# Performance work log

Measured on AMD Instinct MI355X. Metric: run time of the kernel, lower is better.

The kernel has to match this reference:

```python
import jax, jax.numpy as jnp
import numpy as np

EMBED_DIM = 1024
HIDDEN = 4 * EMBED_DIM
BATCH, SEQ = 4, 4096
EPS = 1e-5


def setup_inputs() -> dict:
    key = jax.random.key(0)
    k1, k2, k3 = jax.random.split(key, 3)
    x = jax.random.normal(k1, (BATCH, SEQ, EMBED_DIM), dtype=jnp.float32)
    # Kaiming-ish init scale for linear weights
    w1 = jax.random.normal(k2, (HIDDEN, EMBED_DIM), dtype=jnp.float32) * (1.0 / np.sqrt(EMBED_DIM))
    w2 = jax.random.normal(k3, (EMBED_DIM, HIDDEN), dtype=jnp.float32) * (1.0 / np.sqrt(HIDDEN))
    return {"x": x, "w1": w1, "w2": w2}


def _quant_weight(w):
    # BitNet-b1.58 absmean ternary quantization: clip(round(w/s), -1, 1) * s
    s = jnp.clip(jnp.mean(jnp.abs(w)), EPS, None)
    wq = jnp.clip(jnp.round(w / s), -1.0, 1.0) * s
    # straight-through estimator
    return w + jax.lax.stop_gradient(wq - w)


def _quant_act(x):
    # int8 per-token absmax quantization of activations
    scale = 127.0 / jnp.clip(jnp.max(jnp.abs(x), axis=-1, keepdims=True), EPS, None)
    xq = jnp.clip(jnp.round(x * scale), -128.0, 127.0) / scale
    return x + jax.lax.stop_gradient(xq - x)


def _bitlinear(x, w):
    # x: [..., in], w: [out, in] -> [..., out]
    return jnp.einsum('bsi,oi->bso', _quant_act(x), _quant_weight(w))


def reference(x, w1, w2):
    h = jax.nn.gelu(_bitlinear(x, w1), approximate=False)  # nn.GELU default = exact erf
    return _bitlinear(h, w2)  # dropout is identity in eval / p=0
```

## Files before the change

kernel.cpp:

```cpp
#include <hip/hip_runtime.h>
#include <hip/hip_bf16.h>
#include <cstdint>
#include <cmath>

typedef int intx4 __attribute__((ext_vector_type(4)));
typedef short shortx8 __attribute__((ext_vector_type(8)));

#define EPSQ 1e-5f

__device__ __forceinline__ void async16(const void* g, void* l) {
  __builtin_amdgcn_global_load_lds(
      (const __attribute__((address_space(1))) unsigned int*)(uintptr_t)g,
      (__attribute__((address_space(3))) unsigned int*)(unsigned int)(uintptr_t)l,
      16, 0, 0);
}

__device__ __forceinline__ int q8(float v, float scale, float lo, float hi) {
  return (int)fminf(fmaxf(rintf(v * scale), lo), hi);
}

__device__ __forceinline__ float fast_gelu(float y) {
  const float t = y * 0.70710678118654752f;
  const float x = fabsf(t);
  const float u = __builtin_amdgcn_rcpf(__builtin_fmaf(0.3275911f, x, 1.0f));
  float p = __builtin_fmaf(1.061405429f, u, -1.453152027f);
  p = __builtin_fmaf(p, u, 1.421413741f);
  p = __builtin_fmaf(p, u, -0.284496736f);
  p = __builtin_fmaf(p, u, 0.254829592f);
  p = p * u;
  const float e = __expf(-x * x);
  const float erf_abs = __builtin_fmaf(-p, e, 1.0f);
  const float erf_t = copysignf(erf_abs, t);
  return 0.5f * y * (1.0f + erf_t);
}

__global__ void k_init(float* rowmax, double* sums) {
  int i = blockIdx.x * 256 + threadIdx.x;
  if (i < 16384) rowmax[i] = 0.0f;
  if (i < 2) sums[i] = 0.0;
}

__global__ __launch_bounds__(256) void k_absmean2(const float* __restrict__ W1,
                                                  const float* __restrict__ W2,
                                                  double* __restrict__ sums) {
  __shared__ double wsum[4];
  const int tid = threadIdx.x;
  const int which = blockIdx.x >> 11;
  const float* __restrict__ W = which ? W2 : W1;
  const size_t base = ((size_t)(blockIdx.x & 2047) * 256 + tid) * 8;
  float4 a = *(const float4*)(W + base);
  float4 b = *(const float4*)(W + base + 4);
  float s = fabsf(a.x) + fabsf(a.y) + fabsf(a.z) + fabsf(a.w) +
            fabsf(b.x) + fabsf(b.y) + fabsf(b.z) + fabsf(b.w);
  double d = (double)s;
#pragma unroll
  for (int i = 1; i < 64; i <<= 1) d += __shfl_xor(d, i);
  const int lane = tid & 63, wave = tid >> 6;
  if (lane == 0) wsum[wave] = d;
  __syncthreads();
  if (tid == 0) atomicAdd(sums + which, wsum[0] + wsum[1] + wsum[2] + wsum[3]);
}

__global__ __launch_bounds__(256) void k_quantw2(const float* __restrict__ W1,
                                                 const float* __restrict__ W2,
                                                 signed char* __restrict__ W1Q,
                                                 signed char* __restrict__ W2Q,
                                                 const double* __restrict__ sums) {
  const int which = blockIdx.x >> 11;
  const float* __restrict__ W = which ? W2 : W1;
  signed char* __restrict__ WQ = which ? W2Q : W1Q;
  const float s = fmaxf((float)(sums[which] * (1.0 / 4194304.0)), EPSQ);
  const float inv_s = 1.0f / s;
  const size_t base = ((size_t)(blockIdx.x & 2047) * 256 + threadIdx.x) * 8;
  float4 a = *(const float4*)(W + base);
  float4 b = *(const float4*)(W + base + 4);
  float v[8] = {a.x, a.y, a.z, a.w, b.x, b.y, b.z, b.w};
  unsigned int lo = 0, hi = 0;
#pragma unroll
  for (int j = 0; j < 4; ++j) {
    lo |= ((unsigned int)(q8(v[j], inv_s, -1.f, 1.f) & 0xff)) << (8 * j);
    hi |= ((unsigned int)(q8(v[4 + j], inv_s, -1.f, 1.f) & 0xff)) << (8 * j);
  }
  uint2 o; o.x = lo; o.y = hi;
  *(uint2*)(WQ + base) = o;
}

__global__ __launch_bounds__(256) void k_quantx(const float* __restrict__ X,
                                                signed char* __restrict__ XQ,
                                                float* __restrict__ dqx) {
  __shared__ float wmax[4];
  const int row = blockIdx.x, tid = threadIdx.x;
  const size_t base = (size_t)row * 1024 + tid * 4;
  float4 a = *(const float4*)(X + base);
  float m = fmaxf(fmaxf(fabsf(a.x), fabsf(a.y)), fmaxf(fabsf(a.z), fabsf(a.w)));
#pragma unroll
  for (int i = 1; i < 64; i <<= 1) m = fmaxf(m, __shfl_xor(m, i));
  const int lane = tid & 63, wave = tid >> 6;
  if (lane == 0) wmax[wave] = m;
  __syncthreads();
  m = fmaxf(fmaxf(wmax[0], wmax[1]), fmaxf(wmax[2], wmax[3]));
  m = fmaxf(m, EPSQ);
  const float scale = 127.f / m;
  if (tid == 0) dqx[row] = m * (1.f / 127.f);
  unsigned int p = ((unsigned int)(q8(a.x, scale, -128.f, 127.f) & 0xff)) |
                   ((unsigned int)(q8(a.y, scale, -128.f, 127.f) & 0xff) << 8) |
                   ((unsigned int)(q8(a.z, scale, -128.f, 127.f) & 0xff) << 16) |
                   ((unsigned int)(q8(a.w, scale, -128.f, 127.f) & 0xff) << 24);
  *(unsigned int*)(XQ + base) = p;
}

template <int KB>
__device__ __forceinline__ void gemm_mainloop(const signed char* __restrict__ A,
                                              const signed char* __restrict__ B,
                                              int bm, int bn, int tid, char* lds,
                                              intx4 (&acc)[4][4]) {
  const int wave = tid >> 6, lane = tid & 63;
  const int wm = wave >> 1, wn = wave & 1;
  const int kq = lane >> 4, lc = lane & 15;

  size_t ag[4], bg[4];
#pragma unroll
  for (int i = 0; i < 4; ++i) {
    int gidx = i * 256 + tid;
    int r = gidx >> 3, g = gidx & 7;
    int gs = g ^ (r & 7);
    ag[i] = (size_t)(bm * 128 + r) * KB + gs * 16;
    bg[i] = (size_t)(bn * 128 + r) * KB + gs * 16;
  }
  int aoff[2][4], boff[2][4];
#pragma unroll
  for (int ks = 0; ks < 2; ++ks) {
#pragma unroll
    for (int t = 0; t < 4; ++t) {
      int ra = wm * 64 + t * 16 + lc;
      aoff[ks][t] = ra * 128 + (((ks * 4 + kq) ^ (ra & 7)) << 4);
      int rb = wn * 64 + t * 16 + lc;
      boff[ks][t] = 16384 + rb * 128 + (((ks * 4 + kq) ^ (rb & 7)) << 4);
    }
  }
#pragma unroll
  for (int ti = 0; ti < 4; ++ti)
#pragma unroll
    for (int tj = 0; tj < 4; ++tj) {
      intx4 z = {0, 0, 0, 0};
      acc[ti][tj] = z;
    }

  for (int kt = 0; kt < KB / 128; ++kt) {
    __syncthreads();
    const int k0 = kt * 128;
#pragma unroll
    for (int i = 0; i < 4; ++i) {
      async16(A + ag[i] + k0, lds + i * 4096 + wave * 1024);
      async16(B + bg[i] + k0, lds + 16384 + i * 4096 + wave * 1024);
    }
    asm volatile("s_waitcnt vmcnt(0)" ::: "memory");
    __syncthreads();
#pragma unroll
    for (int ks = 0; ks < 2; ++ks) {
      intx4 af[4], bfr[4];
#pragma unroll
      for (int t = 0; t < 4; ++t) af[t] = *(const intx4*)(lds + aoff[ks][t]);
#pragma unroll
      for (int t = 0; t < 4; ++t) bfr[t] = *(const intx4*)(lds + boff[ks][t]);
#pragma unroll
      for (int ti = 0; ti < 4; ++ti)
#pragma unroll
        for (int tj = 0; tj < 4; ++tj)
          acc[ti][tj] =
              __builtin_amdgcn_mfma_i32_16x16x64_i8(af[ti], bfr[tj], acc[ti][tj], 0, 0, 0);
    }
  }
}

__global__ __launch_bounds__(256) void k_gemm1(const signed char* __restrict__ A,
                                               const signed char* __restrict__ B,
                                               const float* __restrict__ dqx,
                                               const double* __restrict__ sums,
                                               short* __restrict__ HS,
                                               float* __restrict__ mblk,
                                               float* __restrict__ rowmax) {
  __shared__ __attribute__((aligned(16))) char lds[32768];
  const int tid = threadIdx.x;
  const int bm = blockIdx.x, bn = blockIdx.y;

  intx4 acc[4][4];
  gemm_mainloop<1024>(A, B, bm, bn, tid, lds, acc);

  const int wave = tid >> 6, lane = tid & 63;
  const int wm = wave >> 1, wn = wave & 1;
  const int kq = lane >> 4, lc = lane & 15;
  const float s1 = fmaxf((float)(sums[0] * (1.0 / 4194304.0)), EPSQ);

  __syncthreads();
  float* smax = (float*)lds;
  if (tid < 128) smax[tid] = 0.0f;
  __syncthreads();

#pragma unroll
  for (int ti = 0; ti < 4; ++ti) {
#pragma unroll
    for (int r = 0; r < 4; ++r) {
      const int lrow = wm * 64 + ti * 16 + kq * 4 + r;
      const int crow = bm * 128 + lrow;
      const float f = s1 * dqx[crow];
      float mx = 0.f;
#pragma unroll
      for (int tj = 0; tj < 4; ++tj) {
        float y = (float)acc[ti][tj][r] * f;
        float h = fast_gelu(y);
        acc[ti][tj][r] = (int)__float_as_uint(h);
        mx = fmaxf(mx, fabsf(h));
      }
      atomicMax((unsigned int*)&smax[lrow], __float_as_uint(mx));
    }
  }
  __syncthreads();
  if (tid < 128) {
    mblk[(size_t)(bm * 128 + tid) * 32 + bn] = smax[tid];
    atomicMax((unsigned int*)&rowmax[bm * 128 + tid], __float_as_uint(smax[tid]));
  }

#pragma unroll
  for (int ti = 0; ti < 4; ++ti) {
#pragma unroll
    for (int r = 0; r < 4; ++r) {
      const int lrow = wm * 64 + ti * 16 + kq * 4 + r;
      const int crow = bm * 128 + lrow;
      const float sc = 32767.0f / fmaxf(smax[lrow], 1e-30f);
#pragma unroll
      for (int tj = 0; tj < 4; ++tj) {
        const int gcol = bn * 128 + wn * 64 + tj * 16 + lc;
        float h = __uint_as_float((unsigned int)acc[ti][tj][r]);
        int v = (int)fminf(fmaxf(rintf(h * sc), -32767.f), 32767.f);
        HS[(size_t)crow * 4096 + gcol] = (short)v;
      }
    }
  }
}

__global__ __launch_bounds__(256) void k_quanth(const short* __restrict__ HS,
                                                const float* __restrict__ mblk,
                                                const float* __restrict__ rowmax,
                                                signed char* __restrict__ HQ) {
  const size_t gid = (size_t)blockIdx.x * 256 + threadIdx.x;
  const size_t base = gid * 8;
  const int row = (int)(base >> 12);
  const int blk = (int)((base >> 7) & 31);
  const float m = fmaxf(rowmax[row], EPSQ);
  const float fb = mblk[(size_t)row * 32 + blk] * (127.0f / 32767.0f) / m;
  shortx8 s = *(const shortx8*)(HS + base);
  unsigned int lo = 0, hi = 0;
#pragma unroll
  for (int j = 0; j < 4; ++j) {
    lo |= ((unsigned int)(q8((float)s[j], fb, -128.f, 127.f) & 0xff)) << (8 * j);
    hi |= ((unsigned int)(q8((float)s[4 + j], fb, -128.f, 127.f) & 0xff)) << (8 * j);
  }
  uint2 o; o.x = lo; o.y = hi;
  *(uint2*)(HQ + base) = o;
}

__global__ __launch_bounds__(256) void k_gemm2(const signed char* __restrict__ A,
                                               const signed char* __restrict__ B,
                                               const float* __restrict__ rowmax,
                                               const double* __restrict__ sums,
                                               float* __restrict__ OUT) {
  __shared__ __attribute__((aligned(16))) char lds[32768];
  const int tid = threadIdx.x;
  const int bm = blockIdx.x, bn = blockIdx.y;

  intx4 acc[4][4];
  gemm_mainloop<4096>(A, B, bm, bn, tid, lds, acc);

  const int wave = tid >> 6, lane = tid & 63;
  const int wm = wave >> 1, wn = wave & 1;
  const int kq = lane >> 4, lc = lane & 15;
  const float s2 = fmaxf((float)(sums[0] * (1.0 / 4194304.0)), EPSQ);
#pragma unroll
  for (int ti = 0; ti < 4; ++ti) {
#pragma unroll
    for (int r = 0; r < 4; ++r) {
      const int crow = bm * 128 + wm * 64 + ti * 16 + kq * 4 + r;
      const float dqh = fmaxf(rowmax[crow], EPSQ) * (1.f / 127.f);
      const float f = s2 * dqh;
#pragma unroll
      for (int tj = 0; tj < 4; ++tj) {
        const int gcol = bn * 128 + wn * 64 + tj * 16 + lc;
        OUT[(size_t)crow * 1024 + gcol] = (float)acc[ti][tj][r] * f;
      }
    }
  }
}

extern "C" void kernel_launch(void* const* d_in, const int* in_sizes, int n_in,
                              void* d_out, int out_size, void* d_ws, size_t ws_size,
                              hipStream_t stream) {
  const float* X  = (const float*)d_in[0];
  const float* W1 = (const float*)d_in[1];
  const float* W2 = (const float*)d_in[2];
  float* OUT = (float*)d_out;

  char* ws = (char*)d_ws;
  signed char* W1Q = (signed char*)(ws);
  signed char* W2Q = (signed char*)(ws + (4u << 20));
  float* DQX       = (float*)(ws + (8u << 20));
  float* ROWMAX    = (float*)(ws + (8u << 20) + 65536);
  double* SUMS     = (double*)(ws + (8u << 20) + 131072);
  float* MBLK      = (float*)(ws + (9u << 20));
  signed char* HQ  = (signed char*)(ws + (11u << 20));
  const size_t fixed = 75u << 20;
  short* HS = (short*)(ws + fixed);

  signed char* XQ = (signed char*)((char*)d_out + 50331648ull);

  int R = 128;
  const int cands[8] = {16384, 8192, 4096, 2048, 1024, 512, 256, 128};
  for (int i = 0; i < 8; ++i) {
    if (fixed + (size_t)cands[i] * 8192ull <= ws_size) { R = cands[i]; break; }
  }

  hipLaunchKernelGGL(k_init, dim3(64), dim3(256), 0, stream, ROWMAX, SUMS);
  hipLaunchKernelGGL(k_absmean2, dim3(4096), dim3(256), 0, stream, W1, W2, SUMS);
  hipLaunchKernelGGL(k_quantw2, dim3(4096), dim3(256), 0, stream, W1, W2, W1Q, W2Q, SUMS);
  hipLaunchKernelGGL(k_quantx, dim3(16384), dim3(256), 0, stream, X, XQ, DQX);

  const int nchunk = 16384 / R;
  for (int c = 0; c < nchunk; ++c) {
    const int row0 = c * R;
    hipLaunchKernelGGL(k_gemm1, dim3(R / 128, 32), dim3(256), 0, stream,
                       XQ + (size_t)row0 * 1024, W1Q, DQX + row0, SUMS,
                       HS, MBLK + (size_t)row0 * 32, ROWMAX + row0);
    hipLaunchKernelGGL(k_quanth, dim3(R * 2), dim3(256), 0, stream,
                       HS, MBLK + (size_t)row0 * 32, ROWMAX + row0,
                       HQ + (size_t)row0 * 4096);
  }
  hipLaunchKernelGGL(k_gemm2, dim3(128, 8), dim3(256), 0, stream,
                     HQ, W2Q, ROWMAX, SUMS + 1, OUT);
}
```

Measured before the change: 452.9 us.

## Double-buffer GEMM mainloop, pack int16 intermediate layout, wave-reduce row max

The shared GEMM mainloop now uses a K step of 64 with two LDS slots, prefetching the next tile while computing the current one, plus setprio around the MFMAs and a launch-bounds occupancy hint. The gemm1 epilogue reduces the row max with cross-lane shuffles before the LDS atomic, and writes the int16 intermediate with v_cvt_pknorm in a 4-row interleaved layout using 8-byte stores. k_quanth is rewritten for this layout, reading 128 bytes and writing four 16-byte rows per thread. Together these aim to hide global-to-LDS latency and cut scattered 2-byte stores, at the cost of more barriers per K step and a new layout that producer and consumer must agree on.

```diff
diff --git a/kernel.cpp b/kernel.cpp
--- a/kernel.cpp
+++ b/kernel.cpp
@@ -4,7 +4,6 @@
 #include <cmath>
 
 typedef int intx4 __attribute__((ext_vector_type(4)));
-typedef short shortx8 __attribute__((ext_vector_type(8)));
 
 #define EPSQ 1e-5f
 
@@ -17,6 +16,12 @@
 
 __device__ __forceinline__ int q8(float v, float scale, float lo, float hi) {
   return (int)fminf(fmaxf(rintf(v * scale), lo), hi);
+}
+
+__device__ __forceinline__ unsigned int pknorm_i16(float a, float b) {
+  unsigned int r;
+  asm("v_cvt_pknorm_i16_f32 %0, %1, %2" : "=v"(r) : "v"(a), "v"(b));
+  return r;
 }
 
 __device__ __forceinline__ float fast_gelu(float y) {
@@ -117,27 +122,29 @@
   const int wave = tid >> 6, lane = tid & 63;
   const int wm = wave >> 1, wn = wave & 1;
   const int kq = lane >> 4, lc = lane & 15;
-
-  size_t ag[4], bg[4];
+  constexpr int NT = KB / 64;
+
+  size_t goff[4];
+  int lbase[4];
 #pragma unroll
   for (int i = 0; i < 4; ++i) {
-    int gidx = i * 256 + tid;
-    int r = gidx >> 3, g = gidx & 7;
-    int gs = g ^ (r & 7);
-    ag[i] = (size_t)(bm * 128 + r) * KB + gs * 16;
-    bg[i] = (size_t)(bn * 128 + r) * KB + gs * 16;
-  }
-  int aoff[2][4], boff[2][4];
-#pragma unroll
-  for (int ks = 0; ks < 2; ++ks) {
-#pragma unroll
-    for (int t = 0; t < 4; ++t) {
-      int ra = wm * 64 + t * 16 + lc;
-      aoff[ks][t] = ra * 128 + (((ks * 4 + kq) ^ (ra & 7)) << 4);
-      int rb = wn * 64 + t * 16 + lc;
-      boff[ks][t] = 16384 + rb * 128 + (((ks * 4 + kq) ^ (rb & 7)) << 4);
-    }
-  }
+    const int idx = (i & 1) * 256 + tid;
+    const int r = idx >> 2, g = idx & 3;
+    const int gl = g ^ ((r >> 1) & 3);
+    const int rowbase = ((i < 2) ? bm : bn) * 128 + r;
+    goff[i] = (size_t)rowbase * KB + gl * 16;
+    lbase[i] = ((i >= 2) ? 8192 : 0) + (i & 1) * 4096 + wave * 1024;
+  }
+
+  int aoff[4], boff[4];
+#pragma unroll
+  for (int t = 0; t < 4; ++t) {
+    const int ra = wm * 64 + t * 16 + lc;
+    aoff[t] = ra * 64 + ((kq ^ ((ra >> 1) & 3)) << 4);
+    const int rb = wn * 64 + t * 16 + lc;
+    boff[t] = 8192 + rb * 64 + ((kq ^ ((rb >> 1) & 3)) << 4);
+  }
+
 #pragma unroll
   for (int ti = 0; ti < 4; ++ti)
 #pragma unroll
@@ -146,41 +153,52 @@
       acc[ti][tj] = z;
     }
 
-  for (int kt = 0; kt < KB / 128; ++kt) {
-    __syncthreads();
-    const int k0 = kt * 128;
-#pragma unroll
-    for (int i = 0; i < 4; ++i) {
-      async16(A + ag[i] + k0, lds + i * 4096 + wave * 1024);
-      async16(B + bg[i] + k0, lds + 16384 + i * 4096 + wave * 1024);
-    }
-    asm volatile("s_waitcnt vmcnt(0)" ::: "memory");
-    __syncthreads();
-#pragma unroll
-    for (int ks = 0; ks < 2; ++ks) {
-      intx4 af[4], bfr[4];
-#pragma unroll
-      for (int t = 0; t < 4; ++t) af[t] = *(const intx4*)(lds + aoff[ks][t]);
-#pragma unroll
-      for (int t = 0; t < 4; ++t) bfr[t] = *(const intx4*)(lds + boff[ks][t]);
-#pragma unroll
-      for (int ti = 0; ti < 4; ++ti)
-#pragma unroll
-        for (int tj = 0; tj < 4; ++tj)
-          acc[ti][tj] =
-              __builtin_amdgcn_mfma_i32_16x16x64_i8(af[ti], bfr[tj], acc[ti][tj], 0, 0, 0);
-    }
-  }
-}
-
-__global__ __launch_bounds__(256) void k_gemm1(const signed char* __restrict__ A,
-                                               const signed char* __restrict__ B,
-                                               const float* __restrict__ dqx,
-                                               const double* __restrict__ sums,
-                                               short* __restrict__ HS,
-                                               float* __restrict__ mblk,
-                                               float* __restrict__ rowmax) {
+#pragma unroll
+  for (int i = 0; i < 4; ++i)
+    async16(((i < 2) ? A : B) + goff[i], lds + lbase[i]);
+
+  for (int t = 0; t < NT; ++t) {
+    if (t + 1 < NT) {
+      char* nslot = lds + ((t + 1) & 1) * 16384;
+      const size_t k0 = (size_t)(t + 1) * 64;
+#pragma unroll
+      for (int i = 0; i < 4; ++i)
+        async16(((i < 2) ? A : B) + goff[i] + k0, nslot + lbase[i]);
+      asm volatile("s_waitcnt vmcnt(4)" ::: "memory");
+    } else {
+      asm volatile("s_waitcnt vmcnt(0)" ::: "memory");
+    }
+    __builtin_amdgcn_s_barrier();
+    __builtin_amdgcn_sched_barrier(0);
+
+    char* slot = lds + (t & 1) * 16384;
+    intx4 af[4], bfr[4];
+#pragma unroll
+    for (int i = 0; i < 4; ++i) af[i] = *(const intx4*)(slot + aoff[i]);
+#pragma unroll
+    for (int i = 0; i < 4; ++i) bfr[i] = *(const intx4*)(slot + boff[i]);
+    __builtin_amdgcn_s_setprio(1);
+#pragma unroll
+    for (int ti = 0; ti < 4; ++ti)
+#pragma unroll
+      for (int tj = 0; tj < 4; ++tj)
+        acc[ti][tj] =
+            __builtin_amdgcn_mfma_i32_16x16x64_i8(af[ti], bfr[tj], acc[ti][tj], 0, 0, 0);
+    __builtin_amdgcn_s_setprio(0);
+    __builtin_amdgcn_sched_barrier(0);
+    __builtin_amdgcn_s_barrier();
+  }
+}
+
+__global__ __launch_bounds__(256, 3) void k_gemm1(const signed char* __restrict__ A,
+                                                  const signed char* __restrict__ B,
+                                                  const float* __restrict__ dqx,
+                                                  const double* __restrict__ sums,
+                                                  short* __restrict__ HSP,
+                                                  float* __restrict__ mblk,
+                                                  float* __restrict__ rowmax) {
   __shared__ __attribute__((aligned(16))) char lds[32768];
+  __shared__ float smax[128];
   const int tid = threadIdx.x;
   const int bm = blockIdx.x, bn = blockIdx.y;
 
@@ -192,8 +210,6 @@
   const int kq = lane >> 4, lc = lane & 15;
   const float s1 = fmaxf((float)(sums[0] * (1.0 / 4194304.0)), EPSQ);
 
-  __syncthreads();
-  float* smax = (float*)lds;
   if (tid < 128) smax[tid] = 0.0f;
   __syncthreads();
 
@@ -212,7 +228,9 @@
         acc[ti][tj][r] = (int)__float_as_uint(h);
         mx = fmaxf(mx, fabsf(h));
       }
-      atomicMax((unsigned int*)&smax[lrow], __float_as_uint(mx));
+#pragma unroll
+      for (int s = 1; s < 16; s <<= 1) mx = fmaxf(mx, __shfl_xor(mx, s));
+      if (lc == 0) atomicMax((unsigned int*)&smax[lrow], __float_as_uint(mx));
     }
   }
   __syncthreads();
@@ -223,48 +241,74 @@
 
 #pragma unroll
   for (int ti = 0; ti < 4; ++ti) {
-#pragma unroll
-    for (int r = 0; r < 4; ++r) {
-      const int lrow = wm * 64 + ti * 16 + kq * 4 + r;
-      const int crow = bm * 128 + lrow;
-      const float sc = 32767.0f / fmaxf(smax[lrow], 1e-30f);
-#pragma unroll
-      for (int tj = 0; tj < 4; ++tj) {
-        const int gcol = bn * 128 + wn * 64 + tj * 16 + lc;
-        float h = __uint_as_float((unsigned int)acc[ti][tj][r]);
-        int v = (int)fminf(fmaxf(rintf(h * sc), -32767.f), 32767.f);
-        HS[(size_t)crow * 4096 + gcol] = (short)v;
-      }
-    }
-  }
-}
-
-__global__ __launch_bounds__(256) void k_quanth(const short* __restrict__ HS,
+    const int lrow0 = wm * 64 + ti * 16 + kq * 4;
+    const int qr = (bm * 128 + lrow0) >> 2;
+    float inv[4];
+#pragma unroll
+    for (int r = 0; r < 4; ++r)
+      inv[r] = __builtin_amdgcn_rcpf(fmaxf(smax[lrow0 + r], 1e-30f));
+#pragma unroll
+    for (int tj = 0; tj < 4; ++tj) {
+      const int gcol = bn * 128 + wn * 64 + tj * 16 + lc;
+      const float h0 = __uint_as_float((unsigned int)acc[ti][tj][0]) * inv[0];
+      const float h1 = __uint_as_float((unsigned int)acc[ti][tj][1]) * inv[1];
+      const float h2 = __uint_as_float((unsigned int)acc[ti][tj][2]) * inv[2];
+      const float h3 = __uint_as_float((unsigned int)acc[ti][tj][3]) * inv[3];
+      uint2 o;
+      o.x = pknorm_i16(h0, h1);
+      o.y = pknorm_i16(h2, h3);
+      *(uint2*)(HSP + ((size_t)qr * 4096 + gcol) * 4) = o;
+    }
+  }
+}
+
+__global__ __launch_bounds__(256) void k_quanth(const short* __restrict__ HSP,
                                                 const float* __restrict__ mblk,
                                                 const float* __restrict__ rowmax,
                                                 signed char* __restrict__ HQ) {
-  const size_t gid = (size_t)blockIdx.x * 256 + threadIdx.x;
-  const size_t base = gid * 8;
-  const int row = (int)(base >> 12);
-  const int blk = (int)((base >> 7) & 31);
-  const float m = fmaxf(rowmax[row], EPSQ);
-  const float fb = mblk[(size_t)row * 32 + blk] * (127.0f / 32767.0f) / m;
-  shortx8 s = *(const shortx8*)(HS + base);
-  unsigned int lo = 0, hi = 0;
-#pragma unroll
-  for (int j = 0; j < 4; ++j) {
-    lo |= ((unsigned int)(q8((float)s[j], fb, -128.f, 127.f) & 0xff)) << (8 * j);
-    hi |= ((unsigned int)(q8((float)s[4 + j], fb, -128.f, 127.f) & 0xff)) << (8 * j);
-  }
-  uint2 o; o.x = lo; o.y = hi;
-  *(uint2*)(HQ + base) = o;
-}
-
-__global__ __launch_bounds__(256) void k_gemm2(const signed char* __restrict__ A,
-                                               const signed char* __restrict__ B,
-                                               const float* __restrict__ rowmax,
-                                               const double* __restrict__ sums,
-                                               float* __restrict__ OUT) {
+  const int gid = blockIdx.x * 256 + threadIdx.x;
+  const int qr = gid >> 8;
+  const int cg = gid & 255;
+  const int c0 = cg * 16;
+  const int blk = c0 >> 7;
+  const int row0 = qr * 4;
+  float fb[4];
+#pragma unroll
+  for (int r = 0; r < 4; ++r) {
+    const float m = fmaxf(rowmax[row0 + r], EPSQ);
+    fb[r] = mblk[(size_t)(row0 + r) * 32 + blk] * (127.0f / 32767.0f) / m;
+  }
+  const uint4* src = (const uint4*)(HSP + ((size_t)qr * 4096 + c0) * 4);
+  uint4 L[8];
+#pragma unroll
+  for (int j = 0; j < 8; ++j) L[j] = src[j];
+
+  unsigned int out[4][4] = {};
+#pragma unroll
+  for (int j = 0; j < 16; ++j) {
+    const unsigned int u01 = (j & 1) ? L[j >> 1].z : L[j >> 1].x;
+    const unsigned int u23 = (j & 1) ? L[j >> 1].w : L[j >> 1].y;
+    const float s0 = (float)(short)(u01 & 0xffff);
+    const float s1 = (float)(short)(u01 >> 16);
+    const float s2 = (float)(short)(u23 & 0xffff);
+    const float s3 = (float)(short)(u23 >> 16);
+    out[0][j >> 2] |= ((unsigned int)(q8(s0, fb[0], -128.f, 127.f) & 0xff)) << (8 * (j & 3));
+    out[1][j >> 2] |= ((unsigned int)(q8(s1, fb[1], -128.f, 127.f) & 0xff)) << (8 * (j & 3));
+    out[2][j >> 2] |= ((unsigned int)(q8(s2, fb[2], -128.f, 127.f) & 0xff)) << (8 * (j & 3));
+    out[3][j >> 2] |= ((unsigned int)(q8(s3, fb[3], -128.f, 127.f) & 0xff)) << (8 * (j & 3));
+  }
+#pragma unroll
+  for (int r = 0; r < 4; ++r) {
+    uint4 o; o.x = out[r][0]; o.y = out[r][1]; o.z = out[r][2]; o.w = out[r][3];
+    *(uint4*)(HQ + (size_t)(row0 + r) * 4096 + c0) = o;
+  }
+}
+
+__global__ __launch_bounds__(256, 3) void k_gemm2(const signed char* __restrict__ A,
+                                                  const signed char* __restrict__ B,
+                                                  const float* __restrict__ rowmax,
+                                                  const double* __restrict__ sums,
+                                                  float* __restrict__ OUT) {
   __shared__ __attribute__((aligned(16))) char lds[32768];
   const int tid = threadIdx.x;
   const int bm = blockIdx.x, bn = blockIdx.y;
@@ -309,7 +353,7 @@
   float* MBLK      = (float*)(ws + (9u << 20));
   signed char* HQ  = (signed char*)(ws + (11u << 20));
   const size_t fixed = 75u << 20;
-  short* HS = (short*)(ws + fixed);
+  short* HSP = (short*)(ws + fixed);
 
   signed char* XQ = (signed char*)((char*)d_out + 50331648ull);
 
@@ -329,9 +373,9 @@
     const int row0 = c * R;
     hipLaunchKernelGGL(k_gemm1, dim3(R / 128, 32), dim3(256), 0, stream,
                        XQ + (size_t)row0 * 1024, W1Q, DQX + row0, SUMS,
-                       HS, MBLK + (size_t)row0 * 32, ROWMAX + row0);
-    hipLaunchKernelGGL(k_quanth, dim3(R * 2), dim3(256), 0, stream,
-                       HS, MBLK + (size_t)row0 * 32, ROWMAX + row0,
+                       HSP, MBLK + (size_t)row0 * 32, ROWMAX + row0);
+    hipLaunchKernelGGL(k_quanth, dim3(R / 4), dim3(256), 0, stream,
+                       HSP, MBLK + (size_t)row0 * 32, ROWMAX + row0,
                        HQ + (size_t)row0 * 4096);
   }
   hipLaunchKernelGGL(k_gemm2, dim3(128, 8), dim3(256), 0, stream,
```

After: 428.1 us. 1.06x faster.
